# Kernel tuning notes

Hardware: AMD Instinct MI355X
Metric: run time of the kernel (lower is better)

Reference implementation:

```python
import jax, jax.numpy as jnp
import numpy as np

# Blade order: 1 | e0 e1 e2 e3 | e01 e02 e03 e12 e13 e23 | e012 e013 e023 e123 | e0123
GRADE = jnp.array([0, 1, 1, 1, 1, 2, 2, 2, 2, 2, 2, 3, 3, 3, 3, 4])
# Invariant bilinear form <~A B>_0 for signature (+,-,-,-)
METRIC = jnp.array([1., 1., -1., -1., -1., -1., -1., -1., 1., 1., 1., 1., 1., 1., -1., -1.], dtype=jnp.float32)
NUM_HEADS, HID_MV, HID_S = 8, 8, 32


def equi_linear(mv, s, w_mv, w_s2mv, w_mv2s, w_s, b_mv, b_s):
    """Pin(1,3)-equivariant linear layer: grade-projection basis maps + scalar<->grade-0 mixing."""
    w16 = w_mv[:, :, GRADE]  # (out_mv, in_mv, 16): one weight per grade, broadcast over blades
    out_mv = jnp.einsum('oix,...ix->...ox', w16, mv)
    out_mv = out_mv.at[..., 0].add(jnp.einsum('oi,...i->...o', w_s2mv, s) + b_mv)
    out_s = (jnp.einsum('oi,...i->...o', w_s, s)
             + jnp.einsum('oi,...i->...o', w_mv2s, mv[..., 0]) + b_s)
    return out_mv, out_s


def setup_inputs() -> dict:
    key = jax.random.key(0)
    ks = jax.random.split(key, 20)
    B, Nq, Nkv = 4, 2048, 2048
    H, Cm, Cs = NUM_HEADS, HID_MV, HID_S

    def w(k, shape, fan_in):
        return jax.random.normal(k, shape, jnp.float32) / np.sqrt(fan_in).astype(np.float32)

    return {
        'multivectors_kv': jax.random.normal(ks[0], (B, Nkv, 16, 16), jnp.float32),
        'multivectors_q': jax.random.normal(ks[1], (B, Nq, 16, 16), jnp.float32),
        'scalars_kv': jax.random.normal(ks[2], (B, Nkv, 64), jnp.float32),
        'scalars_q': jax.random.normal(ks[3], (B, Nq, 64), jnp.float32),
        # q_linear: 16 mv -> Cm*H=64 mv, 64 s -> Cs*H=256 s
        'wq_mv': w(ks[4], (Cm * H, 16, 5), 16), 'wq_s2mv': w(ks[5], (Cm * H, 64), 64),
        'wq_mv2s': w(ks[6], (Cs * H, 16), 16), 'wq_s': w(ks[7], (Cs * H, 64), 64),
        'bq_mv': jnp.zeros((Cm * H,), jnp.float32), 'bq_s': jnp.zeros((Cs * H,), jnp.float32),
        # kv_linear: 16 mv -> 2*Cm=16 mv, 64 s -> 2*Cs=64 s (multi-query: shared across heads)
        'wkv_mv': w(ks[8], (2 * Cm, 16, 5), 16), 'wkv_s2mv': w(ks[9], (2 * Cm, 64), 64),
        'wkv_mv2s': w(ks[10], (2 * Cs, 16), 16), 'wkv_s': w(ks[11], (2 * Cs, 64), 64),
        'bkv_mv': jnp.zeros((2 * Cm,), jnp.float32), 'bkv_s': jnp.zeros((2 * Cs,), jnp.float32),
        # out_linear: Cm*H=64 mv -> 16 mv, Cs*H=256 s -> 64 s
        'wo_mv': w(ks[12], (16, Cm * H, 5), Cm * H), 'wo_s2mv': w(ks[13], (16, Cs * H), Cs * H),
        'wo_mv2s': w(ks[14], (64, Cm * H), Cm * H), 'wo_s': w(ks[15], (64, Cs * H), Cs * H),
        'bo_mv': jnp.zeros((16,), jnp.float32), 'bo_s': jnp.zeros((64,), jnp.float32),
        'head_scale': jnp.ones((H,), jnp.float32),
    }


def reference(multivectors_kv, multivectors_q, scalars_kv, scalars_q,
              wq_mv, wq_s2mv, wq_mv2s, wq_s, bq_mv, bq_s,
              wkv_mv, wkv_s2mv, wkv_mv2s, wkv_s, bkv_mv, bkv_s,
              wo_mv, wo_s2mv, wo_mv2s, wo_s, bo_mv, bo_s, head_scale):
    B, Nq = multivectors_q.shape[0], multivectors_q.shape[1]
    H, Cm, Cs = NUM_HEADS, HID_MV, HID_S

    q_mv, q_s = equi_linear(multivectors_q, scalars_q, wq_mv, wq_s2mv, wq_mv2s, wq_s, bq_mv, bq_s)
    kv_mv, kv_s = equi_linear(multivectors_kv, scalars_kv, wkv_mv, wkv_s2mv, wkv_mv2s, wkv_s, bkv_mv, bkv_s)
    k_mv, v_mv = jnp.split(kv_mv, 2, axis=-2)  # (B,Nkv,Cm,16) each
    k_s, v_s = jnp.split(kv_s, 2, axis=-1)     # (B,Nkv,Cs) each

    # einops '(hidden num_heads)': hidden is the outer factor
    q_mv = jnp.moveaxis(q_mv.reshape(B, Nq, Cm, H, 16), 3, 1)  # (B,H,Nq,Cm,16)
    q_s = jnp.moveaxis(q_s.reshape(B, Nq, Cs, H), 3, 1)        # (B,H,Nq,Cs)

    scale = np.float32(1.0 / np.sqrt(16 * Cm + Cs))  # flattened feature dim
    scores = (jnp.einsum('bhqcx,bkcx->bhqk', q_mv, k_mv * METRIC)
              + jnp.einsum('bhqs,bks->bhqk', q_s, k_s)) * scale
    attn = jax.nn.softmax(scores, axis=-1)  # (B,H,Nq,Nkv)
    h_mv = jnp.einsum('bhqk,bkcx->bhqcx', attn, v_mv)
    h_s = jnp.einsum('bhqk,bks->bhqs', attn, v_s)

    h_mv = h_mv * head_scale[None, :, None, None, None]
    h_s = h_s * head_scale[None, :, None, None]

    # '(n_heads hidden_channels)': heads outer
    h_mv = jnp.moveaxis(h_mv, 1, 2).reshape(B, Nq, H * Cm, 16)
    h_s = jnp.moveaxis(h_s, 1, 2).reshape(B, Nq, H * Cs)

    return equi_linear(h_mv, h_s, wo_mv, wo_s2mv, wo_mv2s, wo_s, bo_mv, bo_s)
```

## Files before the change

kernel.cpp:

```cpp
#include <hip/hip_runtime.h>
#include <hip/hip_bf16.h>
#include <cstdint>

#define H_  8
#define B_  4
#define NQ  2048
#define NKV 2048
#define DF  160

typedef __attribute__((ext_vector_type(8))) short bf16x8;
typedef __attribute__((ext_vector_type(4))) float f32x4;

__constant__ int   c_grade[16]  = {0,1,1,1,1,2,2,2,2,2,2,3,3,3,3,4};
__constant__ float c_metric[16] = {1.f,1.f,-1.f,-1.f,-1.f,-1.f,-1.f,-1.f,
                                   1.f,1.f,1.f,1.f,1.f,1.f,-1.f,-1.f};

#define SCALE_LOG2E 0.11405506f

__device__ __forceinline__ unsigned short f2bf(float f) {
    union { float f; unsigned u; } v; v.f = f;
    return (unsigned short)((v.u + 0x7FFFu + ((v.u >> 16) & 1u)) >> 16);
}

__global__ __launch_bounds__(256) void expand_wq(
    const float* __restrict__ wmv, const float* __restrict__ ws2mv,
    const float* __restrict__ wmv2s, const float* __restrict__ ws,
    const float* __restrict__ bmv, const float* __restrict__ bs,
    unsigned short* __restrict__ Wq)
{
    const int j = blockIdx.x;
    const int h = j / 160, pos = j % 160;
    for (int k = threadIdx.x; k < 352; k += 256) {
        float val = 0.f;
        if (pos < 128) {
            int c = pos >> 4, x = pos & 15, o = c * 8 + h, g = c_grade[x];
            if (k < 256)       { if ((k & 15) == x) val = wmv[(o*16 + (k>>4))*5 + g]; }
            else if (k < 320)  { if (x == 0) val = ws2mv[o*64 + (k-256)]; }
            else if (k == 320) { if (x == 0) val = bmv[o]; }
        } else {
            int cs = pos - 128, o2 = cs * 8 + h;
            if (k < 256)       { if ((k & 15) == 0) val = wmv2s[o2*16 + (k>>4)]; }
            else if (k < 320)  val = ws[o2*64 + (k-256)];
            else if (k == 320) val = bs[o2];
        }
        Wq[(size_t)j*352 + k] = f2bf(val * SCALE_LOG2E);
    }
}

__global__ __launch_bounds__(256) void expand_wkv(
    const float* __restrict__ wmv, const float* __restrict__ ws2mv,
    const float* __restrict__ wmv2s, const float* __restrict__ ws,
    const float* __restrict__ bmv, const float* __restrict__ bs,
    unsigned short* __restrict__ Wkv)
{
    const int j = blockIdx.x;
    const int side = j / 160, pos = j % 160;
    for (int k = threadIdx.x; k < 352; k += 256) {
        float val = 0.f, mult = 1.f;
        if (pos < 128) {
            int c = pos >> 4, x = pos & 15, o = side * 8 + c, g = c_grade[x];
            if (side == 0) mult = c_metric[x];
            if (k < 256)       { if ((k & 15) == x) val = wmv[(o*16 + (k>>4))*5 + g]; }
            else if (k < 320)  { if (x == 0) val = ws2mv[o*64 + (k-256)]; }
            else if (k == 320) { if (x == 0) val = bmv[o]; }
        } else {
            int s = pos - 128, o2 = side * 32 + s;
            if (k < 256)       { if ((k & 15) == 0) val = wmv2s[o2*16 + (k>>4)]; }
            else if (k < 320)  val = ws[o2*64 + (k-256)];
            else if (k == 320) val = bs[o2];
        }
        Wkv[(size_t)j*352 + k] = f2bf(val * mult);
    }
}

__global__ __launch_bounds__(256) void expand_wo(
    const float* __restrict__ wmv, const float* __restrict__ ws2mv,
    const float* __restrict__ wmv2s, const float* __restrict__ ws,
    const float* __restrict__ bmv, const float* __restrict__ bs,
    unsigned short* __restrict__ Wo)
{
    const int j = blockIdx.x;
    for (int k = threadIdx.x; k < 1408; k += 256) {
        float val = 0.f;
        if (j < 256) {
            int o2 = j >> 4, x = j & 15, g = c_grade[x];
            if (k < 1280) {
                int hh = k / 160, pp = k % 160;
                if (pp < 128) { if ((pp & 15) == x) val = wmv[(o2*64 + hh*8 + (pp>>4))*5 + g]; }
                else          { if (x == 0) val = ws2mv[o2*256 + hh*32 + (pp-128)]; }
            } else if (k == 1280) { if (x == 0) val = bmv[o2]; }
        } else {
            int o2 = j - 256;
            if (k < 1280) {
                int hh = k / 160, pp = k % 160;
                if (pp < 128) { if ((pp & 15) == 0) val = wmv2s[o2*64 + hh*8 + (pp>>4)]; }
                else          val = ws[o2*256 + hh*32 + (pp-128)];
            } else if (k == 1280) val = bs[o2];
        }
        Wo[(size_t)j*1408 + k] = f2bf(val);
    }
}

#define ASTR 360
#define WSTR 40

__global__ __launch_bounds__(256) void gemm_q(
    const float* __restrict__ mvq, const float* __restrict__ sq,
    const unsigned short* __restrict__ Wq, unsigned short* __restrict__ Qbuf)
{
    const int tok0 = blockIdx.x * 64, h = blockIdx.y;
    const int b = tok0 / NQ, n0 = tok0 % NQ;
    const int t = threadIdx.x, w = t >> 6, lane = t & 63, l16 = lane & 15, lq = lane >> 4;

    __shared__ __align__(16) unsigned short Ash[64][ASTR];
    __shared__ __align__(16) unsigned short Wsh[160][WSTR];

    const float4* mv4 = (const float4*)(mvq + (size_t)tok0 * 256);
    const float4* s4  = (const float4*)(sq  + (size_t)tok0 * 64);
    #pragma unroll
    for (int r = 0; r < 20; ++r) {
        int slot = t + 256 * r;
        int tok = slot / 80, q = slot % 80;
        float4 v = (q < 64) ? mv4[tok * 64 + q] : s4[tok * 16 + (q - 64)];
        int col = (q < 64) ? q * 4 : 256 + (q - 64) * 4;
        unsigned lo = (unsigned)f2bf(v.x) | ((unsigned)f2bf(v.y) << 16);
        unsigned hi = (unsigned)f2bf(v.z) | ((unsigned)f2bf(v.w) << 16);
        uint2 u; u.x = lo; u.y = hi;
        *(uint2*)&Ash[tok][col] = u;
    }
    #pragma unroll
    for (int r = 0; r < 9; ++r) {
        int idx = t + 256 * r;
        int tok = idx / 36, cc = idx % 36;
        Ash[tok][320 + cc] = (cc == 0) ? (unsigned short)0x3F80 : (unsigned short)0;
    }
    __syncthreads();

    bf16x8 af[11];
    #pragma unroll
    for (int ks = 0; ks < 11; ++ks)
        af[ks] = *(const bf16x8*)&Ash[w * 16 + l16][ks * 32 + lq * 8];

    f32x4 acc[10];
    #pragma unroll
    for (int nt = 0; nt < 10; ++nt) acc[nt] = f32x4{0.f, 0.f, 0.f, 0.f};

    const unsigned short* Wbase = Wq + (size_t)h * 160 * 352;
    for (int ks = 0; ks < 11; ++ks) {
        __syncthreads();
        #pragma unroll
        for (int r = 0; r < 3; ++r) {
            int s = t + 256 * r;
            if (s < 640) {
                int row = s >> 2, c4 = s & 3;
                *(uint4*)&Wsh[row][c4 * 8] =
                    *(const uint4*)(Wbase + (size_t)row * 352 + ks * 32 + c4 * 8);
            }
        }
        __syncthreads();
        #pragma unroll
        for (int nt = 0; nt < 10; ++nt) {
            bf16x8 wf = *(const bf16x8*)&Wsh[nt * 16 + l16][lq * 8];
            acc[nt] = __builtin_amdgcn_mfma_f32_16x16x32_bf16(af[ks], wf, acc[nt], 0, 0, 0);
        }
    }

    unsigned short* qb = Qbuf + ((size_t)(b * H_ + h) * NQ + n0) * DF;
    #pragma unroll
    for (int nt = 0; nt < 10; ++nt)
        #pragma unroll
        for (int r = 0; r < 4; ++r) {
            int tok = w * 16 + 4 * lq + r;
            qb[(size_t)tok * DF + nt * 16 + l16] = f2bf(acc[nt][r]);
        }
}

__global__ __launch_bounds__(256) void gemm_kv(
    const float* __restrict__ mvkv, const float* __restrict__ skv,
    const unsigned short* __restrict__ Wkv,
    unsigned short* __restrict__ Kbuf, unsigned short* __restrict__ Vtbuf)
{
    const int tok0 = blockIdx.x * 64, slice = blockIdx.y;
    const int b = tok0 / NKV, n0 = tok0 % NKV;
    const int t = threadIdx.x, w = t >> 6, lane = t & 63, l16 = lane & 15, lq = lane >> 4;

    __shared__ __align__(16) unsigned short Ash[64][ASTR];
    __shared__ __align__(16) unsigned short Wsh[160][WSTR];

    const float4* mv4 = (const float4*)(mvkv + (size_t)tok0 * 256);
    const float4* s4  = (const float4*)(skv  + (size_t)tok0 * 64);
    #pragma unroll
    for (int r = 0; r < 20; ++r) {
        int slot = t + 256 * r;
        int tok = slot / 80, q = slot % 80;
        float4 v = (q < 64) ? mv4[tok * 64 + q] : s4[tok * 16 + (q - 64)];
        int col = (q < 64) ? q * 4 : 256 + (q - 64) * 4;
        unsigned lo = (unsigned)f2bf(v.x) | ((unsigned)f2bf(v.y) << 16);
        unsigned hi = (unsigned)f2bf(v.z) | ((unsigned)f2bf(v.w) << 16);
        uint2 u; u.x = lo; u.y = hi;
        *(uint2*)&Ash[tok][col] = u;
    }
    #pragma unroll
    for (int r = 0; r < 9; ++r) {
        int idx = t + 256 * r;
        int tok = idx / 36, cc = idx % 36;
        Ash[tok][320 + cc] = (cc == 0) ? (unsigned short)0x3F80 : (unsigned short)0;
    }
    __syncthreads();

    bf16x8 af[11];
    #pragma unroll
    for (int ks = 0; ks < 11; ++ks)
        af[ks] = *(const bf16x8*)&Ash[w * 16 + l16][ks * 32 + lq * 8];

    f32x4 acc[10];
    #pragma unroll
    for (int nt = 0; nt < 10; ++nt) acc[nt] = f32x4{0.f, 0.f, 0.f, 0.f};

    const unsigned short* Wbase = Wkv + (size_t)slice * 160 * 352;
    for (int ks = 0; ks < 11; ++ks) {
        __syncthreads();
        #pragma unroll
        for (int r = 0; r < 3; ++r) {
            int s = t + 256 * r;
            if (s < 640) {
                int row = s >> 2, c4 = s & 3;
                *(uint4*)&Wsh[row][c4 * 8] =
                    *(const uint4*)(Wbase + (size_t)row * 352 + ks * 32 + c4 * 8);
            }
        }
        __syncthreads();
        #pragma unroll
        for (int nt = 0; nt < 10; ++nt) {
            bf16x8 wf = *(const bf16x8*)&Wsh[nt * 16 + l16][lq * 8];
            acc[nt] = __builtin_amdgcn_mfma_f32_16x16x32_bf16(af[ks], wf, acc[nt], 0, 0, 0);
        }
    }

    if (slice == 0) {
        unsigned short* kb = Kbuf + ((size_t)b * NKV + n0) * DF;
        #pragma unroll
        for (int nt = 0; nt < 10; ++nt)
            #pragma unroll
            for (int r = 0; r < 4; ++r) {
                int tok = w * 16 + 4 * lq + r;
                kb[(size_t)tok * DF + nt * 16 + l16] = f2bf(acc[nt][r]);
            }
    } else {
        unsigned short* vb = Vtbuf + (size_t)b * DF * NKV;
        #pragma unroll
        for (int nt = 0; nt < 10; ++nt) {
            int pos = nt * 16 + l16;
            unsigned lo = (unsigned)f2bf(acc[nt][0]) | ((unsigned)f2bf(acc[nt][1]) << 16);
            unsigned hi = (unsigned)f2bf(acc[nt][2]) | ((unsigned)f2bf(acc[nt][3]) << 16);
            uint2 u; u.x = lo; u.y = hi;
            *(uint2*)(vb + (size_t)pos * NKV + n0 + w * 16 + 4 * lq) = u;
        }
    }
}

__global__ __launch_bounds__(256) void gemm_o(
    const unsigned short* __restrict__ Hb, const unsigned short* __restrict__ Wo,
    float* __restrict__ out)
{
    const int tok0 = blockIdx.x * 64, slice = blockIdx.y;
    const int b = tok0 / NQ, n0 = tok0 % NQ;
    const int t = threadIdx.x, w = t >> 6, lane = t & 63, l16 = lane & 15, lq = lane >> 4;

    __shared__ __align__(16) unsigned short Ash[64][ASTR];
    __shared__ __align__(16) unsigned short Wsh[160][WSTR];

    f32x4 acc[10];
    #pragma unroll
    for (int nt = 0; nt < 10; ++nt) acc[nt] = f32x4{0.f, 0.f, 0.f, 0.f};

    const unsigned short* Wbase = Wo + (size_t)slice * 160 * 1408;

    for (int kc = 0; kc < 4; ++kc) {
        __syncthreads();
        #pragma unroll
        for (int r = 0; r < 11; ++r) {
            int s = t + 256 * r;
            int tok = s / 44, g = s % 44;
            int f0 = kc * 352 + g * 8;
            uint4 val;
            if (f0 < 1280) {
                int hh = f0 / 160, pp = f0 % 160;
                val = *(const uint4*)(Hb + ((size_t)(b * H_ + hh) * NQ + n0 + tok) * DF + pp);
            } else if (f0 == 1280) {
                val.x = 0x3F80u; val.y = 0; val.z = 0; val.w = 0;
            } else {
                val.x = 0; val.y = 0; val.z = 0; val.w = 0;
            }
            *(uint4*)&Ash[tok][g * 8] = val;
        }
        __syncthreads();

        bf16x8 af[11];
        #pragma unroll
        for (int ks = 0; ks < 11; ++ks)
            af[ks] = *(const bf16x8*)&Ash[w * 16 + l16][ks * 32 + lq * 8];

        for (int ks = 0; ks < 11; ++ks) {
            __syncthreads();
            #pragma unroll
            for (int r = 0; r < 3; ++r) {
                int s = t + 256 * r;
                if (s < 640) {
                    int row = s >> 2, c4 = s & 3;
                    *(uint4*)&Wsh[row][c4 * 8] =
                        *(const uint4*)(Wbase + (size_t)row * 1408 + kc * 352 + ks * 32 + c4 * 8);
                }
            }
            __syncthreads();
            #pragma unroll
            for (int nt = 0; nt < 10; ++nt) {
                bf16x8 wf = *(const bf16x8*)&Wsh[nt * 16 + l16][lq * 8];
                acc[nt] = __builtin_amdgcn_mfma_f32_16x16x32_bf16(af[ks], wf, acc[nt], 0, 0, 0);
            }
        }
    }

    const size_t sbase = (size_t)B_ * NQ * 256;
    #pragma unroll
    for (int nt = 0; nt < 10; ++nt) {
        int j = slice * 160 + nt * 16 + l16;
        #pragma unroll
        for (int r = 0; r < 4; ++r) {
            size_t tok = tok0 + w * 16 + 4 * lq + r;
            if (j < 256) out[tok * 256 + j] = acc[nt][r];
            else         out[sbase + tok * 64 + (j - 256)] = acc[nt][r];
        }
    }
}

__global__ __launch_bounds__(256, 2) void attn_kernel(
    const unsigned short* __restrict__ Qb,
    const unsigned short* __restrict__ Kb0,
    const unsigned short* __restrict__ Vb0,
    const float* __restrict__ head_scale,
    unsigned short* __restrict__ Hb)
{
    const int qt = blockIdx.x, hp = blockIdx.y, b = blockIdx.z;
    const int tid  = threadIdx.x;
    const int w    = tid >> 6;
    const int lane = tid & 63;
    const int l16  = lane & 15;
    const int lq   = lane >> 4;
    const int qbase = qt * 64;

    __shared__ __align__(16) unsigned short Ksh[64][168];
    __shared__ __align__(16) unsigned short Vsh[160][72];
    __shared__ __align__(16) unsigned short Psh[2][4][16][72];

    bf16x8 onesf;
    #pragma unroll
    for (int j = 0; j < 8; ++j) onesf[j] = (short)0x3F80;

    bf16x8 qf[2][5];
    #pragma unroll
    for (int s = 0; s < 2; ++s) {
        const unsigned short* qrow =
            Qb + ((size_t)(b * H_ + hp * 2 + s) * NQ + qbase + w * 16 + l16) * DF;
        #pragma unroll
        for (int ks = 0; ks < 5; ++ks)
            qf[s][ks] = *reinterpret_cast<const bf16x8*>(qrow + ks * 32 + lq * 8);
    }

    f32x4 O[2][11];
    #pragma unroll
    for (int s = 0; s < 2; ++s)
        #pragma unroll
        for (int d = 0; d < 11; ++d) O[s][d] = f32x4{0.f, 0.f, 0.f, 0.f};

    const unsigned short* Kb = Kb0 + (size_t)b * NKV * DF;
    const unsigned short* Vb = Vb0 + (size_t)b * DF * NKV;

    for (int kt = 0; kt < NKV / 64; ++kt) {
        __syncthreads();
        #pragma unroll
        for (int c = 0; c < 5; ++c) {
            int idx = tid + c * 256;
            int r = idx / 20, col = idx % 20;
            *reinterpret_cast<uint4*>(&Ksh[r][col * 8]) =
                *reinterpret_cast<const uint4*>(Kb + (size_t)(kt * 64 + r) * DF + col * 8);
        }
        #pragma unroll
        for (int c = 0; c < 5; ++c) {
            int idx = tid + c * 256;
            int r = idx >> 3, col = idx & 7;
            *reinterpret_cast<uint4*>(&Vsh[r][col * 8]) =
                *reinterpret_cast<const uint4*>(Vb + (size_t)r * NKV + kt * 64 + col * 8);
        }
        __syncthreads();

        f32x4 sc[2][4];
        #pragma unroll
        for (int nt = 0; nt < 4; ++nt) {
            sc[0][nt] = f32x4{0.f, 0.f, 0.f, 0.f};
            sc[1][nt] = f32x4{0.f, 0.f, 0.f, 0.f};
            #pragma unroll
            for (int ks = 0; ks < 5; ++ks) {
                bf16x8 kf = *reinterpret_cast<const bf16x8*>(
                    &Ksh[nt * 16 + l16][ks * 32 + lq * 8]);
                sc[0][nt] = __builtin_amdgcn_mfma_f32_16x16x32_bf16(qf[0][ks], kf, sc[0][nt], 0, 0, 0);
                sc[1][nt] = __builtin_amdgcn_mfma_f32_16x16x32_bf16(qf[1][ks], kf, sc[1][nt], 0, 0, 0);
            }
        }

        #pragma unroll
        for (int s = 0; s < 2; ++s)
            #pragma unroll
            for (int nt = 0; nt < 4; ++nt)
                #pragma unroll
                for (int r = 0; r < 4; ++r)
                    Psh[s][w][lq * 4 + r][nt * 16 + l16] =
                        f2bf(__builtin_amdgcn_exp2f(sc[s][nt][r]));

        #pragma unroll
        for (int k2 = 0; k2 < 2; ++k2) {
            bf16x8 pf0 = *reinterpret_cast<const bf16x8*>(&Psh[0][w][l16][k2 * 32 + lq * 8]);
            bf16x8 pf1 = *reinterpret_cast<const bf16x8*>(&Psh[1][w][l16][k2 * 32 + lq * 8]);
            O[0][10] = __builtin_amdgcn_mfma_f32_16x16x32_bf16(pf0, onesf, O[0][10], 0, 0, 0);
            O[1][10] = __builtin_amdgcn_mfma_f32_16x16x32_bf16(pf1, onesf, O[1][10], 0, 0, 0);
            #pragma unroll
            for (int d = 0; d < 10; ++d) {
                bf16x8 vf = *reinterpret_cast<const bf16x8*>(
                    &Vsh[d * 16 + l16][k2 * 32 + lq * 8]);
                O[0][d] = __builtin_amdgcn_mfma_f32_16x16x32_bf16(pf0, vf, O[0][d], 0, 0, 0);
                O[1][d] = __builtin_amdgcn_mfma_f32_16x16x32_bf16(pf1, vf, O[1][d], 0, 0, 0);
            }
        }
    }

    #pragma unroll
    for (int s = 0; s < 2; ++s) {
        float hsc = head_scale[hp * 2 + s];
        #pragma unroll
        for (int r = 0; r < 4; ++r) {
            float inv = hsc / O[s][10][r];
            int qrow = qbase + w * 16 + lq * 4 + r;
            unsigned short* orow =
                Hb + ((size_t)(b * H_ + hp * 2 + s) * NQ + qrow) * DF;
            #pragma unroll
            for (int d = 0; d < 10; ++d)
                orow[d * 16 + l16] = f2bf(O[s][d][r] * inv);
        }
    }
}

extern "C" void kernel_launch(void* const* d_in, const int* in_sizes, int n_in,
                              void* d_out, int out_size, void* d_ws, size_t ws_size,
                              hipStream_t stream) {
    const float* mv_kv  = (const float*)d_in[0];
    const float* mv_q   = (const float*)d_in[1];
    const float* s_kv   = (const float*)d_in[2];
    const float* s_q    = (const float*)d_in[3];
    const float* wq_mv  = (const float*)d_in[4];
    const float* wq_s2mv= (const float*)d_in[5];
    const float* wq_mv2s= (const float*)d_in[6];
    const float* wq_s   = (const float*)d_in[7];
    const float* bq_mv  = (const float*)d_in[8];
    const float* bq_s   = (const float*)d_in[9];
    const float* wkv_mv = (const float*)d_in[10];
    const float* wkv_s2mv=(const float*)d_in[11];
    const float* wkv_mv2s=(const float*)d_in[12];
    const float* wkv_s  = (const float*)d_in[13];
    const float* bkv_mv = (const float*)d_in[14];
    const float* bkv_s  = (const float*)d_in[15];
    const float* wo_mv  = (const float*)d_in[16];
    const float* wo_s2mv= (const float*)d_in[17];
    const float* wo_mv2s= (const float*)d_in[18];
    const float* wo_s   = (const float*)d_in[19];
    const float* bo_mv  = (const float*)d_in[20];
    const float* bo_s   = (const float*)d_in[21];
    const float* head_scale = (const float*)d_in[22];

    char* ws = (char*)d_ws;
    unsigned short* Qbuf  = (unsigned short*)(ws);
    unsigned short* Kbuf  = (unsigned short*)(ws + 20971520);
    unsigned short* Vtbuf = (unsigned short*)(ws + 23592960);
    unsigned short* Hbuf  = (unsigned short*)(ws + 26214400);
    unsigned short* Wq    = (unsigned short*)(ws + 47185920);
    unsigned short* Wkv   = (unsigned short*)(ws + 48087040);
    unsigned short* Wo    = (unsigned short*)(ws + 48312320);

    expand_wq <<<1280, 256, 0, stream>>>(wq_mv, wq_s2mv, wq_mv2s, wq_s, bq_mv, bq_s, Wq);
    expand_wkv<<<320, 256, 0, stream>>>(wkv_mv, wkv_s2mv, wkv_mv2s, wkv_s, bkv_mv, bkv_s, Wkv);
    expand_wo <<<320, 256, 0, stream>>>(wo_mv, wo_s2mv, wo_mv2s, wo_s, bo_mv, bo_s, Wo);

    gemm_q <<<dim3(128, 8), 256, 0, stream>>>(mv_q, s_q, Wq, Qbuf);
    gemm_kv<<<dim3(128, 2), 256, 0, stream>>>(mv_kv, s_kv, Wkv, Kbuf, Vtbuf);

    dim3 g3(NQ / 64, H_ / 2, B_);
    attn_kernel<<<g3, 256, 0, stream>>>(Qbuf, Kbuf, Vtbuf, head_scale, Hbuf);

    gemm_o<<<dim3(128, 2), 256, 0, stream>>>(Hbuf, Wo, (float*)d_out);
}
```

Baseline: 332.2 us.

## Merge weight-expansion kernels and read GEMM weights directly from global memory

Combines the three weight-expansion launches into one kernel writing a contiguous Wqkv buffer. The projection GEMMs drop LDS staging of weight tiles and the per-k-step barriers, instead loading B fragments straight from global memory (likely L2-resident). Each gemm_q block now processes four heads and each gemm_kv block both K and V, so the staged activation tile is reused across more outputs and the grids shrink. The trade-off is fewer blocks and uncoalesced global fragment loads that depend on cache hits.

```diff
diff --git a/kernel.cpp b/kernel.cpp
--- a/kernel.cpp
+++ b/kernel.cpp
@@ -22,98 +22,90 @@
     return (unsigned short)((v.u + 0x7FFFu + ((v.u >> 16) & 1u)) >> 16);
 }
 
-__global__ __launch_bounds__(256) void expand_wq(
-    const float* __restrict__ wmv, const float* __restrict__ ws2mv,
-    const float* __restrict__ wmv2s, const float* __restrict__ ws,
-    const float* __restrict__ bmv, const float* __restrict__ bs,
-    unsigned short* __restrict__ Wq)
+__global__ __launch_bounds__(256) void expand_all(
+    const float* __restrict__ qmv,  const float* __restrict__ qs2mv,
+    const float* __restrict__ qmv2s,const float* __restrict__ qws,
+    const float* __restrict__ qbmv, const float* __restrict__ qbs,
+    const float* __restrict__ kmv,  const float* __restrict__ ks2mv,
+    const float* __restrict__ kmv2s,const float* __restrict__ kws,
+    const float* __restrict__ kbmv, const float* __restrict__ kbs,
+    const float* __restrict__ omv,  const float* __restrict__ os2mv,
+    const float* __restrict__ omv2s,const float* __restrict__ ows,
+    const float* __restrict__ obmv, const float* __restrict__ obs,
+    unsigned short* __restrict__ Wqkv, unsigned short* __restrict__ Wo)
 {
     const int j = blockIdx.x;
-    const int h = j / 160, pos = j % 160;
-    for (int k = threadIdx.x; k < 352; k += 256) {
-        float val = 0.f;
-        if (pos < 128) {
-            int c = pos >> 4, x = pos & 15, o = c * 8 + h, g = c_grade[x];
-            if (k < 256)       { if ((k & 15) == x) val = wmv[(o*16 + (k>>4))*5 + g]; }
-            else if (k < 320)  { if (x == 0) val = ws2mv[o*64 + (k-256)]; }
-            else if (k == 320) { if (x == 0) val = bmv[o]; }
-        } else {
-            int cs = pos - 128, o2 = cs * 8 + h;
-            if (k < 256)       { if ((k & 15) == 0) val = wmv2s[o2*16 + (k>>4)]; }
-            else if (k < 320)  val = ws[o2*64 + (k-256)];
-            else if (k == 320) val = bs[o2];
-        }
-        Wq[(size_t)j*352 + k] = f2bf(val * SCALE_LOG2E);
-    }
-}
-
-__global__ __launch_bounds__(256) void expand_wkv(
-    const float* __restrict__ wmv, const float* __restrict__ ws2mv,
-    const float* __restrict__ wmv2s, const float* __restrict__ ws,
-    const float* __restrict__ bmv, const float* __restrict__ bs,
-    unsigned short* __restrict__ Wkv)
+    if (j < 1280) {
+        const int h = j / 160, pos = j % 160;
+        for (int k = threadIdx.x; k < 352; k += 256) {
+            float val = 0.f;
+            if (pos < 128) {
+                int c = pos >> 4, x = pos & 15, o = c * 8 + h, g = c_grade[x];
+                if (k < 256)       { if ((k & 15) == x) val = qmv[(o*16 + (k>>4))*5 + g]; }
+                else if (k < 320)  { if (x == 0) val = qs2mv[o*64 + (k-256)]; }
+                else if (k == 320) { if (x == 0) val = qbmv[o]; }
+            } else {
+                int cs = pos - 128, o2 = cs * 8 + h;
+                if (k < 256)       { if ((k & 15) == 0) val = qmv2s[o2*16 + (k>>4)]; }
+                else if (k < 320)  val = qws[o2*64 + (k-256)];
+                else if (k == 320) val = qbs[o2];
+            }
+            Wqkv[(size_t)j*352 + k] = f2bf(val * SCALE_LOG2E);
+        }
+    } else if (j < 1600) {
+        const int jj = j - 1280;
+        const int side = jj / 160, pos = jj % 160;
+        for (int k = threadIdx.x; k < 352; k += 256) {
+            float val = 0.f, mult = 1.f;
+            if (pos < 128) {
+                int c = pos >> 4, x = pos & 15, o = side * 8 + c, g = c_grade[x];
+                if (side == 0) mult = c_metric[x];
+                if (k < 256)       { if ((k & 15) == x) val = kmv[(o*16 + (k>>4))*5 + g]; }
+                else if (k < 320)  { if (x == 0) val = ks2mv[o*64 + (k-256)]; }
+                else if (k == 320) { if (x == 0) val = kbmv[o]; }
+            } else {
+                int s = pos - 128, o2 = side * 32 + s;
+                if (k < 256)       { if ((k & 15) == 0) val = kmv2s[o2*16 + (k>>4)]; }
+                else if (k < 320)  val = kws[o2*64 + (k-256)];
+                else if (k == 320) val = kbs[o2];
+            }
+            Wqkv[(size_t)j*352 + k] = f2bf(val * mult);
+        }
+    } else {
+        const int jj = j - 1600;
+        for (int k = threadIdx.x; k < 1408; k += 256) {
+            float val = 0.f;
+            if (jj < 256) {
+                int o2 = jj >> 4, x = jj & 15, g = c_grade[x];
+                if (k < 1280) {
+                    int hh = k / 160, pp = k % 160;
+                    if (pp < 128) { if ((pp & 15) == x) val = omv[(o2*64 + hh*8 + (pp>>4))*5 + g]; }
+                    else          { if (x == 0) val = os2mv[o2*256 + hh*32 + (pp-128)]; }
+                } else if (k == 1280) { if (x == 0) val = obmv[o2]; }
+            } else {
+                int o2 = jj - 256;
+                if (k < 1280) {
+                    int hh = k / 160, pp = k % 160;
+                    if (pp < 128) { if ((pp & 15) == 0) val = omv2s[o2*64 + hh*8 + (pp>>4)]; }
+                    else          val = ows[o2*256 + hh*32 + (pp-128)];
+                } else if (k == 1280) val = obs[o2];
+            }
+            Wo[(size_t)jj*1408 + k] = f2bf(val);
+        }
+    }
+}
+
+#define ASTR 360
+
+__global__ __launch_bounds__(256, 2) void gemm_q(
+    const float* __restrict__ mvq, const float* __restrict__ sq,
+    const unsigned short* __restrict__ Wqkv, unsigned short* __restrict__ Qbuf)
 {
-    const int j = blockIdx.x;
-    const int side = j / 160, pos = j % 160;
-    for (int k = threadIdx.x; k < 352; k += 256) {
-        float val = 0.f, mult = 1.f;
-        if (pos < 128) {
-            int c = pos >> 4, x = pos & 15, o = side * 8 + c, g = c_grade[x];
-            if (side == 0) mult = c_metric[x];
-            if (k < 256)       { if ((k & 15) == x) val = wmv[(o*16 + (k>>4))*5 + g]; }
-            else if (k < 320)  { if (x == 0) val = ws2mv[o*64 + (k-256)]; }
-            else if (k == 320) { if (x == 0) val = bmv[o]; }
-        } else {
-            int s = pos - 128, o2 = side * 32 + s;
-            if (k < 256)       { if ((k & 15) == 0) val = wmv2s[o2*16 + (k>>4)]; }
-            else if (k < 320)  val = ws[o2*64 + (k-256)];
-            else if (k == 320) val = bs[o2];
-        }
-        Wkv[(size_t)j*352 + k] = f2bf(val * mult);
-    }
-}
-
-__global__ __launch_bounds__(256) void expand_wo(
-    const float* __restrict__ wmv, const float* __restrict__ ws2mv,
-    const float* __restrict__ wmv2s, const float* __restrict__ ws,
-    const float* __restrict__ bmv, const float* __restrict__ bs,
-    unsigned short* __restrict__ Wo)
-{
-    const int j = blockIdx.x;
-    for (int k = threadIdx.x; k < 1408; k += 256) {
-        float val = 0.f;
-        if (j < 256) {
-            int o2 = j >> 4, x = j & 15, g = c_grade[x];
-            if (k < 1280) {
-                int hh = k / 160, pp = k % 160;
-                if (pp < 128) { if ((pp & 15) == x) val = wmv[(o2*64 + hh*8 + (pp>>4))*5 + g]; }
-                else          { if (x == 0) val = ws2mv[o2*256 + hh*32 + (pp-128)]; }
-            } else if (k == 1280) { if (x == 0) val = bmv[o2]; }
-        } else {
-            int o2 = j - 256;
-            if (k < 1280) {
-                int hh = k / 160, pp = k % 160;
-                if (pp < 128) { if ((pp & 15) == 0) val = wmv2s[o2*64 + hh*8 + (pp>>4)]; }
-                else          val = ws[o2*256 + hh*32 + (pp-128)];
-            } else if (k == 1280) val = bs[o2];
-        }
-        Wo[(size_t)j*1408 + k] = f2bf(val);
-    }
-}
-
-#define ASTR 360
-#define WSTR 40
-
-__global__ __launch_bounds__(256) void gemm_q(
-    const float* __restrict__ mvq, const float* __restrict__ sq,
-    const unsigned short* __restrict__ Wq, unsigned short* __restrict__ Qbuf)
-{
-    const int tok0 = blockIdx.x * 64, h = blockIdx.y;
+    const int tok0 = blockIdx.x * 64, half = blockIdx.y;
     const int b = tok0 / NQ, n0 = tok0 % NQ;
     const int t = threadIdx.x, w = t >> 6, lane = t & 63, l16 = lane & 15, lq = lane >> 4;
 
     __shared__ __align__(16) unsigned short Ash[64][ASTR];
-    __shared__ __align__(16) unsigned short Wsh[160][WSTR];
 
     const float4* mv4 = (const float4*)(mvq + (size_t)tok0 * 256);
     const float4* s4  = (const float4*)(sq  + (size_t)tok0 * 64);
@@ -141,51 +133,39 @@
     for (int ks = 0; ks < 11; ++ks)
         af[ks] = *(const bf16x8*)&Ash[w * 16 + l16][ks * 32 + lq * 8];
 
-    f32x4 acc[10];
-    #pragma unroll
-    for (int nt = 0; nt < 10; ++nt) acc[nt] = f32x4{0.f, 0.f, 0.f, 0.f};
-
-    const unsigned short* Wbase = Wq + (size_t)h * 160 * 352;
-    for (int ks = 0; ks < 11; ++ks) {
-        __syncthreads();
-        #pragma unroll
-        for (int r = 0; r < 3; ++r) {
-            int s = t + 256 * r;
-            if (s < 640) {
-                int row = s >> 2, c4 = s & 3;
-                *(uint4*)&Wsh[row][c4 * 8] =
-                    *(const uint4*)(Wbase + (size_t)row * 352 + ks * 32 + c4 * 8);
-            }
-        }
-        __syncthreads();
-        #pragma unroll
-        for (int nt = 0; nt < 10; ++nt) {
-            bf16x8 wf = *(const bf16x8*)&Wsh[nt * 16 + l16][lq * 8];
-            acc[nt] = __builtin_amdgcn_mfma_f32_16x16x32_bf16(af[ks], wf, acc[nt], 0, 0, 0);
-        }
-    }
-
-    unsigned short* qb = Qbuf + ((size_t)(b * H_ + h) * NQ + n0) * DF;
-    #pragma unroll
-    for (int nt = 0; nt < 10; ++nt)
-        #pragma unroll
-        for (int r = 0; r < 4; ++r) {
-            int tok = w * 16 + 4 * lq + r;
-            qb[(size_t)tok * DF + nt * 16 + l16] = f2bf(acc[nt][r]);
-        }
-}
-
-__global__ __launch_bounds__(256) void gemm_kv(
+    #pragma unroll
+    for (int g = 0; g < 4; ++g) {
+        const int h = half * 4 + g;
+        const unsigned short* Wb = Wqkv + (size_t)h * 160 * 352;
+        f32x4 acc[10];
+        #pragma unroll
+        for (int nt = 0; nt < 10; ++nt) acc[nt] = f32x4{0.f, 0.f, 0.f, 0.f};
+        #pragma unroll
+        for (int ks = 0; ks < 11; ++ks)
+            #pragma unroll
+            for (int nt = 0; nt < 10; ++nt) {
+                bf16x8 wf = *(const bf16x8*)(Wb + (size_t)(nt * 16 + l16) * 352 + ks * 32 + lq * 8);
+                acc[nt] = __builtin_amdgcn_mfma_f32_16x16x32_bf16(af[ks], wf, acc[nt], 0, 0, 0);
+            }
+        unsigned short* qb = Qbuf + ((size_t)(b * H_ + h) * NQ + n0) * DF;
+        #pragma unroll
+        for (int nt = 0; nt < 10; ++nt)
+            #pragma unroll
+            for (int r = 0; r < 4; ++r)
+                qb[(size_t)(w * 16 + 4 * lq + r) * DF + nt * 16 + l16] = f2bf(acc[nt][r]);
+    }
+}
+
+__global__ __launch_bounds__(256, 2) void gemm_kv(
     const float* __restrict__ mvkv, const float* __restrict__ skv,
-    const unsigned short* __restrict__ Wkv,
+    const unsigned short* __restrict__ Wqkv,
     unsigned short* __restrict__ Kbuf, unsigned short* __restrict__ Vtbuf)
 {
-    const int tok0 = blockIdx.x * 64, slice = blockIdx.y;
+    const int tok0 = blockIdx.x * 64;
     const int b = tok0 / NKV, n0 = tok0 % NKV;
     const int t = threadIdx.x, w = t >> 6, lane = t & 63, l16 = lane & 15, lq = lane >> 4;
 
     __shared__ __align__(16) unsigned short Ash[64][ASTR];
-    __shared__ __align__(16) unsigned short Wsh[160][WSTR];
 
     const float4* mv4 = (const float4*)(mvkv + (size_t)tok0 * 256);
     const float4* s4  = (const float4*)(skv  + (size_t)tok0 * 64);
@@ -213,68 +193,53 @@
     for (int ks = 0; ks < 11; ++ks)
         af[ks] = *(const bf16x8*)&Ash[w * 16 + l16][ks * 32 + lq * 8];
 
-    f32x4 acc[10];
-    #pragma unroll
-    for (int nt = 0; nt < 10; ++nt) acc[nt] = f32x4{0.f, 0.f, 0.f, 0.f};
-
-    const unsigned short* Wbase = Wkv + (size_t)slice * 160 * 352;
-    for (int ks = 0; ks < 11; ++ks) {
-        __syncthreads();
-        #pragma unroll
-        for (int r = 0; r < 3; ++r) {
-            int s = t + 256 * r;
-            if (s < 640) {
-                int row = s >> 2, c4 = s & 3;
-                *(uint4*)&Wsh[row][c4 * 8] =
-                    *(const uint4*)(Wbase + (size_t)row * 352 + ks * 32 + c4 * 8);
-            }
-        }
-        __syncthreads();
-        #pragma unroll
-        for (int nt = 0; nt < 10; ++nt) {
-            bf16x8 wf = *(const bf16x8*)&Wsh[nt * 16 + l16][lq * 8];
-            acc[nt] = __builtin_amdgcn_mfma_f32_16x16x32_bf16(af[ks], wf, acc[nt], 0, 0, 0);
-        }
-    }
-
-    if (slice == 0) {
-        unsigned short* kb = Kbuf + ((size_t)b * NKV + n0) * DF;
-        #pragma unroll
-        for (int nt = 0; nt < 10; ++nt)
-            #pragma unroll
-            for (int r = 0; r < 4; ++r) {
-                int tok = w * 16 + 4 * lq + r;
-                kb[(size_t)tok * DF + nt * 16 + l16] = f2bf(acc[nt][r]);
-            }
-    } else {
-        unsigned short* vb = Vtbuf + (size_t)b * DF * NKV;
-        #pragma unroll
-        for (int nt = 0; nt < 10; ++nt) {
-            int pos = nt * 16 + l16;
-            unsigned lo = (unsigned)f2bf(acc[nt][0]) | ((unsigned)f2bf(acc[nt][1]) << 16);
-            unsigned hi = (unsigned)f2bf(acc[nt][2]) | ((unsigned)f2bf(acc[nt][3]) << 16);
-            uint2 u; u.x = lo; u.y = hi;
-            *(uint2*)(vb + (size_t)pos * NKV + n0 + w * 16 + 4 * lq) = u;
-        }
-    }
-}
-
-__global__ __launch_bounds__(256) void gemm_o(
+    #pragma unroll
+    for (int g = 0; g < 2; ++g) {
+        const unsigned short* Wb = Wqkv + (size_t)(1280 + g * 160) * 352;
+        f32x4 acc[10];
+        #pragma unroll
+        for (int nt = 0; nt < 10; ++nt) acc[nt] = f32x4{0.f, 0.f, 0.f, 0.f};
+        #pragma unroll
+        for (int ks = 0; ks < 11; ++ks)
+            #pragma unroll
+            for (int nt = 0; nt < 10; ++nt) {
+                bf16x8 wf = *(const bf16x8*)(Wb + (size_t)(nt * 16 + l16) * 352 + ks * 32 + lq * 8);
+                acc[nt] = __builtin_amdgcn_mfma_f32_16x16x32_bf16(af[ks], wf, acc[nt], 0, 0, 0);
+            }
+        if (g == 0) {
+            unsigned short* kb = Kbuf + ((size_t)b * NKV + n0) * DF;
+            #pragma unroll
+            for (int nt = 0; nt < 10; ++nt)
+                #pragma unroll
+                for (int r = 0; r < 4; ++r)
+                    kb[(size_t)(w * 16 + 4 * lq + r) * DF + nt * 16 + l16] = f2bf(acc[nt][r]);
+        } else {
+            unsigned short* vb = Vtbuf + (size_t)b * DF * NKV;
+            #pragma unroll
+            for (int nt = 0; nt < 10; ++nt) {
+                int pos = nt * 16 + l16;
+                unsigned lo = (unsigned)f2bf(acc[nt][0]) | ((unsigned)f2bf(acc[nt][1]) << 16);
+                unsigned hi = (unsigned)f2bf(acc[nt][2]) | ((unsigned)f2bf(acc[nt][3]) << 16);
+                uint2 u; u.x = lo; u.y = hi;
+                *(uint2*)(vb + (size_t)pos * NKV + n0 + w * 16 + 4 * lq) = u;
+            }
+        }
+    }
+}
+
+__global__ __launch_bounds__(256, 2) void gemm_o(
     const unsigned short* __restrict__ Hb, const unsigned short* __restrict__ Wo,
     float* __restrict__ out)
 {
-    const int tok0 = blockIdx.x * 64, slice = blockIdx.y;
+    const int tok0 = blockIdx.x * 64, half = blockIdx.y;
     const int b = tok0 / NQ, n0 = tok0 % NQ;
     const int t = threadIdx.x, w = t >> 6, lane = t & 63, l16 = lane & 15, lq = lane >> 4;
 
     __shared__ __align__(16) unsigned short Ash[64][ASTR];
-    __shared__ __align__(16) unsigned short Wsh[160][WSTR];
 
     f32x4 acc[10];
     #pragma unroll
     for (int nt = 0; nt < 10; ++nt) acc[nt] = f32x4{0.f, 0.f, 0.f, 0.f};
-
-    const unsigned short* Wbase = Wo + (size_t)slice * 160 * 1408;
 
     for (int kc = 0; kc < 4; ++kc) {
         __syncthreads();
@@ -301,30 +266,20 @@
         for (int ks = 0; ks < 11; ++ks)
             af[ks] = *(const bf16x8*)&Ash[w * 16 + l16][ks * 32 + lq * 8];
 
-        for (int ks = 0; ks < 11; ++ks) {
-            __syncthreads();
-            #pragma unroll
-            for (int r = 0; r < 3; ++r) {
-                int s = t + 256 * r;
-                if (s < 640) {
-                    int row = s >> 2, c4 = s & 3;
-                    *(uint4*)&Wsh[row][c4 * 8] =
-                        *(const uint4*)(Wbase + (size_t)row * 1408 + kc * 352 + ks * 32 + c4 * 8);
-                }
-            }
-            __syncthreads();
+        #pragma unroll
+        for (int ks = 0; ks < 11; ++ks)
             #pragma unroll
             for (int nt = 0; nt < 10; ++nt) {
-                bf16x8 wf = *(const bf16x8*)&Wsh[nt * 16 + l16][lq * 8];
+                bf16x8 wf = *(const bf16x8*)(
+                    Wo + (size_t)(half * 160 + nt * 16 + l16) * 1408 + kc * 352 + ks * 32 + lq * 8);
                 acc[nt] = __builtin_amdgcn_mfma_f32_16x16x32_bf16(af[ks], wf, acc[nt], 0, 0, 0);
             }
-        }
     }
 
     const size_t sbase = (size_t)B_ * NQ * 256;
     #pragma unroll
     for (int nt = 0; nt < 10; ++nt) {
-        int j = slice * 160 + nt * 16 + l16;
+        int j = half * 160 + nt * 16 + l16;
         #pragma unroll
         for (int r = 0; r < 4; ++r) {
             size_t tok = tok0 + w * 16 + 4 * lq + r;
@@ -481,16 +436,16 @@
     unsigned short* Kbuf  = (unsigned short*)(ws + 20971520);
     unsigned short* Vtbuf = (unsigned short*)(ws + 23592960);
     unsigned short* Hbuf  = (unsigned short*)(ws + 26214400);
-    unsigned short* Wq    = (unsigned short*)(ws + 47185920);
-    unsigned short* Wkv   = (unsigned short*)(ws + 48087040);
+    unsigned short* Wqkv  = (unsigned short*)(ws + 47185920);
     unsigned short* Wo    = (unsigned short*)(ws + 48312320);
 
-    expand_wq <<<1280, 256, 0, stream>>>(wq_mv, wq_s2mv, wq_mv2s, wq_s, bq_mv, bq_s, Wq);
-    expand_wkv<<<320, 256, 0, stream>>>(wkv_mv, wkv_s2mv, wkv_mv2s, wkv_s, bkv_mv, bkv_s, Wkv);
-    expand_wo <<<320, 256, 0, stream>>>(wo_mv, wo_s2mv, wo_mv2s, wo_s, bo_mv, bo_s, Wo);
-
-    gemm_q <<<dim3(128, 8), 256, 0, stream>>>(mv_q, s_q, Wq, Qbuf);
-    gemm_kv<<<dim3(128, 2), 256, 0, stream>>>(mv_kv, s_kv, Wkv, Kbuf, Vtbuf);
+    expand_all<<<1920, 256, 0, stream>>>(
+        wq_mv, wq_s2mv, wq_mv2s, wq_s, bq_mv, bq_s,
+        wkv_mv, wkv_s2mv, wkv_mv2s, wkv_s, bkv_mv, bkv_s,
+        wo_mv, wo_s2mv, wo_mv2s, wo_s, bo_mv, bo_s, Wqkv, Wo);
+
+    gemm_q <<<dim3(128, 2), 256, 0, stream>>>(mv_q, s_q, Wqkv, Qbuf);
+    gemm_kv<<<128, 256, 0, stream>>>(mv_kv, s_kv, Wqkv, Kbuf, Vtbuf);
 
     dim3 g3(NQ / 64, H_ / 2, B_);
     attn_kernel<<<g3, 256, 0, stream>>>(Qbuf, Kbuf, Vtbuf, head_scale, Hbuf);
```

New measurement: 434.9 us. +30.9%, slower.
